# Kernel optimization log

Hardware: AMD Instinct MI355X
Metric: run time of the kernel (lower is better)

The kernel has to match this reference:

```python
import jax, jax.numpy as jnp
import numpy as np

B, H, W = 64, 512, 512


def setup_inputs() -> dict:
    key = jax.random.key(0)
    k1, k2 = jax.random.split(key)
    t1 = jax.random.normal(k1, (B, H, W), dtype=jnp.float32)
    t2 = jax.random.normal(k2, (B, H, W), dtype=jnp.float32)
    return {"t1": t1, "t2": t2}


def _wass_p2(a, b):
    # a, b: [H, W] -> flatten to empirical distributions of N values each
    av = a.reshape(-1)
    bv = b.reshape(-1)
    n = av.shape[0]
    a_sorted = jnp.sort(av)
    b_sorted = jnp.sort(bv)
    all_values = jnp.sort(jnp.concatenate([av, bv]))  # [2N]
    deltas = jnp.diff(all_values)                      # [2N-1]
    q = all_values[:-1]
    # right-side searchsorted == count of values <= q  (empirical CDF * N)
    i1 = jnp.searchsorted(a_sorted, q, side="right")
    i2 = jnp.searchsorted(b_sorted, q, side="right")
    c1 = i1.astype(jnp.float32) / n
    c2 = i2.astype(jnp.float32) / n
    # p = 2 branch of the original loss
    return jnp.sqrt(jnp.sum(jnp.square(c1 - c2) * deltas))


def reference(t1, t2):
    losses = jax.vmap(_wass_p2)(t1, t2)  # [B]
    return jnp.mean(losses)
```

## Files before the change

kernel.cpp:

```cpp
#include <hip/hip_runtime.h>
#include <stdint.h>

#define LOG_N   18
#define N_PER   262144
#define BATCHES 64
#define NBINS   4096
#define HALFB   2048
#define HTPB    512
#define SPLITS  16
#define CHUNK   (N_PER / SPLITS)
#define SLICEW  (NBINS / 2)
#define GTPB    512
#define BPT     (NBINS / GTPB)

__device__ __forceinline__ uint32_t f2k(float f) {
    uint32_t u = __float_as_uint(f);
    uint32_t m = (uint32_t)((int32_t)u >> 31) | 0x80000000u;
    return (u ^ m) >> 16;
}
__device__ __forceinline__ uint32_t comp(uint32_t k) {
    bool pos = (k >= 0x8000u);
    int  c   = pos ? ((int)k - 0xB900 + HALFB) : ((int)k - 0x3F00);
    int  lo  = pos ? HALFB : 0;
    int  hi  = lo + HALFB - 1;
    c = c < lo ? lo : c;
    c = c > hi ? hi : c;
    return (uint32_t)c;
}
__device__ __forceinline__ float binEdge(uint32_t c) {
    uint32_t k = (c < HALFB) ? (0x3F00u + c) : (0xB900u + (c - HALFB));
    uint32_t x = k << 16;
    uint32_t u = (x & 0x80000000u) ? (x ^ 0x80000000u) : ~x;
    return __uint_as_float(u);
}

__global__ __launch_bounds__(HTPB) void hist_kernel(
        const float* __restrict__ t1, const float* __restrict__ t2,
        uint32_t* __restrict__ slices) {
    __shared__ uint32_t h[NBINS];
    int tid  = threadIdx.x;
    int tile = blockIdx.x;
    int bat  = tile / SPLITS;
    int part = tile % SPLITS;
    {
        uint4 z; z.x = z.y = z.z = z.w = 0u;
        uint4* h4 = (uint4*)h;
        h4[tid] = z; h4[tid + HTPB] = z;
    }
    __syncthreads();
    size_t boff = ((size_t)bat << LOG_N) + (size_t)part * CHUNK;
    const float4* pA = (const float4*)(t1 + boff);
    const float4* pB = (const float4*)(t2 + boff);
#pragma unroll
    for (int k = 0; k < 2; ++k) {
        float4 a0 = pA[tid + (4 * k + 0) * HTPB];
        float4 a1 = pA[tid + (4 * k + 1) * HTPB];
        float4 a2 = pA[tid + (4 * k + 2) * HTPB];
        float4 a3 = pA[tid + (4 * k + 3) * HTPB];
        atomicAdd(&h[comp(f2k(a0.x))], 1u); atomicAdd(&h[comp(f2k(a0.y))], 1u);
        atomicAdd(&h[comp(f2k(a0.z))], 1u); atomicAdd(&h[comp(f2k(a0.w))], 1u);
        atomicAdd(&h[comp(f2k(a1.x))], 1u); atomicAdd(&h[comp(f2k(a1.y))], 1u);
        atomicAdd(&h[comp(f2k(a1.z))], 1u); atomicAdd(&h[comp(f2k(a1.w))], 1u);
        atomicAdd(&h[comp(f2k(a2.x))], 1u); atomicAdd(&h[comp(f2k(a2.y))], 1u);
        atomicAdd(&h[comp(f2k(a2.z))], 1u); atomicAdd(&h[comp(f2k(a2.w))], 1u);
        atomicAdd(&h[comp(f2k(a3.x))], 1u); atomicAdd(&h[comp(f2k(a3.y))], 1u);
        atomicAdd(&h[comp(f2k(a3.z))], 1u); atomicAdd(&h[comp(f2k(a3.w))], 1u);
    }
#pragma unroll
    for (int k = 0; k < 2; ++k) {
        float4 b0 = pB[tid + (4 * k + 0) * HTPB];
        float4 b1 = pB[tid + (4 * k + 1) * HTPB];
        float4 b2 = pB[tid + (4 * k + 2) * HTPB];
        float4 b3 = pB[tid + (4 * k + 3) * HTPB];
        atomicAdd(&h[comp(f2k(b0.x))], (uint32_t)-1); atomicAdd(&h[comp(f2k(b0.y))], (uint32_t)-1);
        atomicAdd(&h[comp(f2k(b0.z))], (uint32_t)-1); atomicAdd(&h[comp(f2k(b0.w))], (uint32_t)-1);
        atomicAdd(&h[comp(f2k(b1.x))], (uint32_t)-1); atomicAdd(&h[comp(f2k(b1.y))], (uint32_t)-1);
        atomicAdd(&h[comp(f2k(b1.z))], (uint32_t)-1); atomicAdd(&h[comp(f2k(b1.w))], (uint32_t)-1);
        atomicAdd(&h[comp(f2k(b2.x))], (uint32_t)-1); atomicAdd(&h[comp(f2k(b2.y))], (uint32_t)-1);
        atomicAdd(&h[comp(f2k(b2.z))], (uint32_t)-1); atomicAdd(&h[comp(f2k(b2.w))], (uint32_t)-1);
        atomicAdd(&h[comp(f2k(b3.x))], (uint32_t)-1); atomicAdd(&h[comp(f2k(b3.y))], (uint32_t)-1);
        atomicAdd(&h[comp(f2k(b3.z))], (uint32_t)-1); atomicAdd(&h[comp(f2k(b3.w))], (uint32_t)-1);
    }
    __syncthreads();
    {
        const uint4* h4 = (const uint4*)h;
        uint4* gs4 = (uint4*)(slices + (size_t)tile * SLICEW);
        uint4 a = h4[2 * tid], b = h4[2 * tid + 1];
        uint4 o;
        o.x = (a.x & 0xFFFFu) | (a.y << 16);
        o.y = (a.z & 0xFFFFu) | (a.w << 16);
        o.z = (b.x & 0xFFFFu) | (b.y << 16);
        o.w = (b.z & 0xFFFFu) | (b.w << 16);
        gs4[tid] = o;
    }
}

__global__ __launch_bounds__(GTPB) void integ_kernel(
        const uint32_t* __restrict__ slices, double* losses) {
    __shared__ short sdiff[NBINS];
    __shared__ int sa[GTPB], sb[GTPB];
    __shared__ double red[GTPB];
    int bl  = blockIdx.x;
    int tid = threadIdx.x;
    const uint4* S4 = (const uint4*)(slices + (size_t)bl * SPLITS * SLICEW);
    const int W4 = SLICEW / 4;

    {
        int d[8];
#pragma unroll
        for (int i = 0; i < 8; ++i) d[i] = 0;
#pragma unroll
        for (int s = 0; s < SPLITS; ++s) {
            uint4 v = S4[s * W4 + tid];
            d[0] += (int)(short)(v.x & 0xFFFFu); d[1] += (int)(short)(v.x >> 16);
            d[2] += (int)(short)(v.y & 0xFFFFu); d[3] += (int)(short)(v.y >> 16);
            d[4] += (int)(short)(v.z & 0xFFFFu); d[5] += (int)(short)(v.z >> 16);
            d[6] += (int)(short)(v.w & 0xFFFFu); d[7] += (int)(short)(v.w >> 16);
        }
#pragma unroll
        for (int i = 0; i < 8; ++i) sdiff[8 * tid + i] = (short)d[i];
    }
    __syncthreads();

    int k0 = tid * BPT;
    int diffs[BPT];
    int s = 0;
#pragma unroll
    for (int k = 0; k < BPT; ++k) { int d = sdiff[k0 + k]; diffs[k] = d; s += d; }
    sa[tid] = s;
    __syncthreads();
    int* cur = sa; int* nxt = sb;
    for (int off = 1; off < GTPB; off <<= 1) {
        int v = cur[tid] + ((tid >= off) ? cur[tid - off] : 0);
        nxt[tid] = v;
        __syncthreads();
        int* tmp = cur; cur = nxt; nxt = tmp;
    }
    int D = tid ? cur[tid - 1] : 0;

    double acc = 0.0;
    float vprev = binEdge((uint32_t)k0);
#pragma unroll
    for (int k = 0; k < BPT; ++k) {
        D += diffs[k];
        float vnext = binEdge((uint32_t)(k0 + k + 1));
        if (D) { double dd = (double)D; acc += dd * dd * (double)(vnext - vprev); }
        vprev = vnext;
    }
    red[tid] = acc;
    __syncthreads();
    for (int off = GTPB / 2; off > 0; off >>= 1) {
        if (tid < off) red[tid] += red[tid + off];
        __syncthreads();
    }
    if (tid == 0) {
        const double inv = 1.0 / ((double)N_PER * (double)N_PER);
        losses[bl] = sqrt(red[0] * inv);
    }
}

__global__ void final_kernel(const double* losses, float* out) {
    int tid = threadIdx.x;
    double loss = losses[tid];
    for (int off = 32; off > 0; off >>= 1)
        loss += __shfl_down(loss, off);
    if (tid == 0) out[0] = (float)(loss / (double)BATCHES);
}

extern "C" void kernel_launch(void* const* d_in, const int* in_sizes, int n_in,
                              void* d_out, int out_size, void* d_ws, size_t ws_size,
                              hipStream_t stream) {
    const float* t1 = (const float*)d_in[0];
    const float* t2 = (const float*)d_in[1];
    float* out = (float*)d_out;

    char* ws = (char*)d_ws;
    double*   losses = (double*)ws;
    uint32_t* slices = (uint32_t*)(ws + 1024);
    size_t need = 1024 + (size_t)BATCHES * SPLITS * SLICEW * 4;
    if (ws_size < need) return;

    hipLaunchKernelGGL(hist_kernel, dim3(BATCHES * SPLITS), dim3(HTPB), 0, stream,
                       t1, t2, slices);
    hipLaunchKernelGGL(integ_kernel, dim3(BATCHES), dim3(GTPB), 0, stream,
                       slices, losses);
    hipLaunchKernelGGL(final_kernel, dim3(1), dim3(BATCHES), 0, stream, losses, out);
}
```

Measured before the change: 32.88 us.

## Split per-batch integration across four blocks using histogram quarter subtotals

The histogram kernel now also emits per-quarter subtotals of each slice's signed bin counts. The integration kernel runs four blocks per batch instead of one, each taking a quarter of the bins and seeding its prefix with the summed subtotals of earlier quarters. Partial squared sums are combined with a double atomicAdd, and the sqrt moves into the final kernel. This raises integration-stage parallelism from 64 blocks to 256, at the cost of an extra memset launch and atomics.

```diff
diff --git a/kernel.cpp b/kernel.cpp
--- a/kernel.cpp
+++ b/kernel.cpp
@@ -10,8 +10,8 @@
 #define SPLITS  16
 #define CHUNK   (N_PER / SPLITS)
 #define SLICEW  (NBINS / 2)
-#define GTPB    512
-#define BPT     (NBINS / GTPB)
+#define QBINS   1024
+#define GTPB    256
 
 __device__ __forceinline__ uint32_t f2k(float f) {
     uint32_t u = __float_as_uint(f);
@@ -36,8 +36,9 @@
 
 __global__ __launch_bounds__(HTPB) void hist_kernel(
         const float* __restrict__ t1, const float* __restrict__ t2,
-        uint32_t* __restrict__ slices) {
+        uint32_t* __restrict__ slices, int* __restrict__ subtot) {
     __shared__ uint32_t h[NBINS];
+    __shared__ int ssub[8];
     int tid  = threadIdx.x;
     int tile = blockIdx.x;
     int bat  = tile / SPLITS;
@@ -82,10 +83,11 @@
         atomicAdd(&h[comp(f2k(b3.z))], (uint32_t)-1); atomicAdd(&h[comp(f2k(b3.w))], (uint32_t)-1);
     }
     __syncthreads();
+    uint4 a, b;
     {
         const uint4* h4 = (const uint4*)h;
+        a = h4[2 * tid]; b = h4[2 * tid + 1];
         uint4* gs4 = (uint4*)(slices + (size_t)tile * SLICEW);
-        uint4 a = h4[2 * tid], b = h4[2 * tid + 1];
         uint4 o;
         o.x = (a.x & 0xFFFFu) | (a.y << 16);
         o.y = (a.z & 0xFFFFu) | (a.w << 16);
@@ -93,41 +95,52 @@
         o.w = (b.z & 0xFFFFu) | (b.w << 16);
         gs4[tid] = o;
     }
+    {
+        int s = (int)a.x + (int)a.y + (int)a.z + (int)a.w
+              + (int)b.x + (int)b.y + (int)b.z + (int)b.w;
+        int lane = tid & 63, wv = tid >> 6;
+#pragma unroll
+        for (int off = 32; off > 0; off >>= 1) s += __shfl_down(s, off);
+        if (lane == 0) ssub[wv] = s;
+        __syncthreads();
+        if (tid < 4) subtot[tile * 4 + tid] = ssub[2 * tid] + ssub[2 * tid + 1];
+    }
 }
 
 __global__ __launch_bounds__(GTPB) void integ_kernel(
-        const uint32_t* __restrict__ slices, double* losses) {
-    __shared__ short sdiff[NBINS];
+        const uint32_t* __restrict__ slices, const int* __restrict__ subtot,
+        double* loss2) {
     __shared__ int sa[GTPB], sb[GTPB];
     __shared__ double red[GTPB];
-    int bl  = blockIdx.x;
+    __shared__ int sDs;
+    int blk = blockIdx.x;
+    int bat = blk >> 2;
+    int q   = blk & 3;
     int tid = threadIdx.x;
-    const uint4* S4 = (const uint4*)(slices + (size_t)bl * SPLITS * SLICEW);
-    const int W4 = SLICEW / 4;
-
-    {
-        int d[8];
-#pragma unroll
-        for (int i = 0; i < 8; ++i) d[i] = 0;
-#pragma unroll
-        for (int s = 0; s < SPLITS; ++s) {
-            uint4 v = S4[s * W4 + tid];
-            d[0] += (int)(short)(v.x & 0xFFFFu); d[1] += (int)(short)(v.x >> 16);
-            d[2] += (int)(short)(v.y & 0xFFFFu); d[3] += (int)(short)(v.y >> 16);
-            d[4] += (int)(short)(v.z & 0xFFFFu); d[5] += (int)(short)(v.z >> 16);
-            d[6] += (int)(short)(v.w & 0xFFFFu); d[7] += (int)(short)(v.w >> 16);
+
+    {
+        int v = 0;
+        if (tid < 16 * q) {
+            int s_ = tid & 15, qp = tid >> 4;
+            v = subtot[(bat * SPLITS + s_) * 4 + qp];
         }
-#pragma unroll
-        for (int i = 0; i < 8; ++i) sdiff[8 * tid + i] = (short)d[i];
-    }
-    __syncthreads();
-
-    int k0 = tid * BPT;
-    int diffs[BPT];
-    int s = 0;
-#pragma unroll
-    for (int k = 0; k < BPT; ++k) { int d = sdiff[k0 + k]; diffs[k] = d; s += d; }
-    sa[tid] = s;
+        if (tid < 64) {
+#pragma unroll
+            for (int off = 32; off > 0; off >>= 1) v += __shfl_down(v, off);
+            if (tid == 0) sDs = v;
+        }
+        __syncthreads();
+    }
+
+    const uint32_t* S = slices + (size_t)bat * SPLITS * SLICEW + q * (QBINS / 2);
+    int d0 = 0, d1 = 0, d2 = 0, d3 = 0;
+#pragma unroll
+    for (int s = 0; s < SPLITS; ++s) {
+        uint2 v = *(const uint2*)(S + (size_t)s * SLICEW + 2 * tid);
+        d0 += (int)(short)(v.x & 0xFFFFu); d1 += (int)(short)(v.x >> 16);
+        d2 += (int)(short)(v.y & 0xFFFFu); d3 += (int)(short)(v.y >> 16);
+    }
+    sa[tid] = d0 + d1 + d2 + d3;
     __syncthreads();
     int* cur = sa; int* nxt = sb;
     for (int off = 1; off < GTPB; off <<= 1) {
@@ -136,32 +149,31 @@
         __syncthreads();
         int* tmp = cur; cur = nxt; nxt = tmp;
     }
-    int D = tid ? cur[tid - 1] : 0;
-
+    int D = sDs + (tid ? cur[tid - 1] : 0);
+
+    uint32_t k0 = (uint32_t)(q * QBINS + 4 * tid);
+    float e0 = binEdge(k0), e1 = binEdge(k0 + 1), e2 = binEdge(k0 + 2);
+    float e3 = binEdge(k0 + 3), e4 = binEdge(k0 + 4);
     double acc = 0.0;
-    float vprev = binEdge((uint32_t)k0);
-#pragma unroll
-    for (int k = 0; k < BPT; ++k) {
-        D += diffs[k];
-        float vnext = binEdge((uint32_t)(k0 + k + 1));
-        if (D) { double dd = (double)D; acc += dd * dd * (double)(vnext - vprev); }
-        vprev = vnext;
-    }
+    D += d0; { double dd = (double)D; acc += dd * dd * (double)(e1 - e0); }
+    D += d1; { double dd = (double)D; acc += dd * dd * (double)(e2 - e1); }
+    D += d2; { double dd = (double)D; acc += dd * dd * (double)(e3 - e2); }
+    D += d3; { double dd = (double)D; acc += dd * dd * (double)(e4 - e3); }
+
     red[tid] = acc;
     __syncthreads();
     for (int off = GTPB / 2; off > 0; off >>= 1) {
         if (tid < off) red[tid] += red[tid + off];
         __syncthreads();
     }
-    if (tid == 0) {
-        const double inv = 1.0 / ((double)N_PER * (double)N_PER);
-        losses[bl] = sqrt(red[0] * inv);
-    }
-}
-
-__global__ void final_kernel(const double* losses, float* out) {
+    if (tid == 0) atomicAdd(&loss2[bat], red[0]);
+}
+
+__global__ void final_kernel(const double* loss2, float* out) {
     int tid = threadIdx.x;
-    double loss = losses[tid];
+    const double inv = 1.0 / ((double)N_PER * (double)N_PER);
+    double loss = sqrt(loss2[tid] * inv);
+#pragma unroll
     for (int off = 32; off > 0; off >>= 1)
         loss += __shfl_down(loss, off);
     if (tid == 0) out[0] = (float)(loss / (double)BATCHES);
@@ -175,14 +187,16 @@
     float* out = (float*)d_out;
 
     char* ws = (char*)d_ws;
-    double*   losses = (double*)ws;
-    uint32_t* slices = (uint32_t*)(ws + 1024);
-    size_t need = 1024 + (size_t)BATCHES * SPLITS * SLICEW * 4;
+    double*   loss2  = (double*)ws;
+    int*      subtot = (int*)(ws + 512);
+    uint32_t* slices = (uint32_t*)(ws + 32768);
+    size_t need = 32768 + (size_t)BATCHES * SPLITS * SLICEW * 4;
     if (ws_size < need) return;
 
+    hipMemsetAsync(loss2, 0, BATCHES * sizeof(double), stream);
     hipLaunchKernelGGL(hist_kernel, dim3(BATCHES * SPLITS), dim3(HTPB), 0, stream,
-                       t1, t2, slices);
-    hipLaunchKernelGGL(integ_kernel, dim3(BATCHES), dim3(GTPB), 0, stream,
-                       slices, losses);
-    hipLaunchKernelGGL(final_kernel, dim3(1), dim3(BATCHES), 0, stream, losses, out);
-}
+                       t1, t2, slices, subtot);
+    hipLaunchKernelGGL(integ_kernel, dim3(BATCHES * 4), dim3(GTPB), 0, stream,
+                       slices, subtot, loss2);
+    hipLaunchKernelGGL(final_kernel, dim3(1), dim3(64), 0, stream, loss2, out);
+}
```

Result: slower. 37.94 us (+15.4%).
